# Kernel optimization log

Hardware: AMD Instinct MI355X
Metric: run time of the kernel (lower is better)

The kernel has to match this reference:

```python
import jax, jax.numpy as jnp
import numpy as np

N_USERS = 50000
N_ITEMS = 50000
E = 400000
S = 128   # in_feats_s (memory / GRU hidden)
T = 64    # in_feats_t (time encoding dim)
ED = 64   # edge feature dim
M = 2 * S + T + ED  # in_feats_m = 384

_BASIS_FREQ = jnp.asarray(1.0 / 10 ** np.linspace(0, 9, T), dtype=jnp.float32)


def time_encode(ts):
    # cos(ts * freq + phase), phase == 0
    return jnp.cos(ts[:, None] * _BASIS_FREQ[None, :])


def mean_message(src_mem, dst_mem, ts, e, src, dst, n_dst):
    # mail per edge: [E, 2S + T + ED]
    mail = jnp.concatenate(
        [src_mem[src], dst_mem[dst], time_encode(ts), e], axis=1)
    s = jax.ops.segment_sum(mail, dst, num_segments=n_dst)
    cnt = jax.ops.segment_sum(jnp.ones_like(ts), dst, num_segments=n_dst)
    return s / jnp.maximum(cnt, 1.0)[:, None]


def gru_step(x, h, w_ih, w_hh, b_ih, b_hh):
    # single-step PyTorch GRU; gate order r, z, n
    gi = x @ w_ih.T + b_ih
    gh = h @ w_hh.T + b_hh
    ir, iz, i_n = jnp.split(gi, 3, axis=1)
    hr, hz, h_n = jnp.split(gh, 3, axis=1)
    r = jax.nn.sigmoid(ir + hr)
    z = jax.nn.sigmoid(iz + hz)
    n = jnp.tanh(i_n + r * h_n)
    return (1.0 - z) * n + z * h


def setup_inputs() -> dict:
    key = jax.random.key(0)
    ks = jax.random.split(key, 16)
    sc = 1.0 / np.sqrt(S)
    return {
        "si":   jax.random.normal(ks[0], (N_USERS, S), jnp.float32),
        "sj":   jax.random.normal(ks[1], (N_ITEMS, S), jnp.float32),
        "si_r": jax.random.normal(ks[2], (N_ITEMS, S), jnp.float32),
        "sj_r": jax.random.normal(ks[3], (N_USERS, S), jnp.float32),
        "t":    jax.random.uniform(ks[4], (E,), jnp.float32),
        "t_r":  jax.random.uniform(ks[5], (E,), jnp.float32),
        "e":    jax.random.normal(ks[6], (E, ED), jnp.float32),
        "e_r":  jax.random.normal(ks[7], (E, ED), jnp.float32),
        "w_ih": jax.random.normal(ks[8], (3 * S, M), jnp.float32) * sc,
        "w_hh": jax.random.normal(ks[9], (3 * S, S), jnp.float32) * sc,
        "b_ih": jax.random.normal(ks[10], (3 * S,), jnp.float32) * sc,
        "b_hh": jax.random.normal(ks[11], (3 * S,), jnp.float32) * sc,
        "src_g":  jax.random.randint(ks[12], (E,), 0, N_USERS, jnp.int32),
        "dst_g":  jax.random.randint(ks[13], (E,), 0, N_ITEMS, jnp.int32),
        "src_gr": jax.random.randint(ks[14], (E,), 0, N_ITEMS, jnp.int32),
        "dst_gr": jax.random.randint(ks[15], (E,), 0, N_USERS, jnp.int32),
    }


def reference(si, sj, si_r, sj_r, t, t_r, e, e_r,
              w_ih, w_hh, b_ih, b_hh,
              src_g, dst_g, src_gr, dst_gr):
    # g: user -> item; g_r: item -> user
    mj = mean_message(si, sj, t, e, src_g, dst_g, N_ITEMS)       # messages to items
    mi = mean_message(si_r, sj_r, t_r, e_r, src_gr, dst_gr, N_USERS)  # messages to users
    si_out = gru_step(mi, sj_r, w_ih, w_hh, b_ih, b_hh)  # user memory update
    sj_out = gru_step(mj, sj, w_ih, w_hh, b_ih, b_hh)    # item memory update
    return (si_out, sj_out)
```

## Files before the change

### kernel.cpp

```cpp
#include <hip/hip_runtime.h>
#include <math.h>

#define NUSERS 50000
#define NITEMS 50000
#define NTOT   100000
#define NNODE  50000
#define NCHUNK 196
#define MTILES 6250
#define KDIM   512

typedef __attribute__((ext_vector_type(4))) float f32x4;
typedef __attribute__((ext_vector_type(8))) short short8;
typedef unsigned int u32;

#define AS1 __attribute__((address_space(1)))
#define AS3 __attribute__((address_space(3)))

static __device__ __forceinline__ unsigned short f2bf(float f) {
  unsigned int u = __float_as_uint(f);
  u += 0x7fffu + ((u >> 16) & 1u);
  return (unsigned short)(u >> 16);
}

static __device__ __forceinline__ void gload_lds16(const void* g, void* l) {
  __builtin_amdgcn_global_load_lds((const AS1 u32*)g, (AS3 u32*)l, 16, 0, 0);
}

__global__ void pack_w_kernel(const float* __restrict__ w_ih,
                              const float* __restrict__ w_hh,
                              const float* __restrict__ b_ih,
                              const float* __restrict__ b_hh,
                              unsigned short* __restrict__ Wb,
                              float* __restrict__ bb) {
  int idx = blockIdx.x * 256 + threadIdx.x;
  int j = idx & 7, l = (idx >> 3) & 63, ktt = idx >> 9;
  int kt = ktt & 15, tt = ktt >> 4;
  int g = tt * 16 + (l & 15);
  int k = kt * 32 + (l >> 4) * 8 + j;
  float v;
  if (g < 256)      v = (k < 384) ? w_ih[g * 384 + k] : w_hh[g * 128 + (k - 384)];
  else if (g < 384) v = (k < 384) ? w_ih[g * 384 + k] : 0.0f;
  else              v = (k < 384) ? 0.0f : w_hh[(g - 128) * 128 + (k - 384)];
  Wb[idx] = f2bf(v);
  if (idx < 512) {
    float b = (idx < 256) ? (b_ih[idx] + b_hh[idx])
            : (idx < 384) ? b_ih[idx]
                          : b_hh[idx - 128];
    bb[idx] = b;
  }
}

__global__ void hist_kernel(const int* __restrict__ dst_g,
                            const int* __restrict__ dst_gr,
                            int* __restrict__ deg_j, int* __restrict__ deg_i, int E) {
  int i = blockIdx.x * 256 + threadIdx.x;
  if (i < E) atomicAdd(&deg_j[dst_g[i]], 1);
  else if (i < 2 * E) atomicAdd(&deg_i[dst_gr[i - E]], 1);
}

__global__ void chunksum_kernel(const int* __restrict__ deg_j,
                                const int* __restrict__ deg_i,
                                int* __restrict__ csum) {
  int c = blockIdx.x;
  const int* deg = (c < NCHUNK) ? deg_j : deg_i;
  int cc = (c < NCHUNK) ? c : c - NCHUNK;
  int t = threadIdx.x;
  int idx = cc * 256 + t;
  int v = (idx < NNODE) ? deg[idx] : 0;
  for (int off = 32; off; off >>= 1) v += __shfl_down(v, off, 64);
  __shared__ int wsum[4];
  if ((t & 63) == 0) wsum[t >> 6] = v;
  __syncthreads();
  if (t == 0) csum[c] = wsum[0] + wsum[1] + wsum[2] + wsum[3];
}

__global__ void chunkscan_kernel(const int* __restrict__ csum, int* __restrict__ coff) {
  int d = blockIdx.x;
  const int* cs = csum + d * NCHUNK;
  int* co = coff + d * NCHUNK;
  int t = threadIdx.x, lane = t & 63, w = t >> 6;
  int v = (t < NCHUNK) ? cs[t] : 0;
  int x = v;
  for (int off = 1; off < 64; off <<= 1) {
    int y = __shfl_up(x, off, 64);
    if (lane >= off) x += y;
  }
  __shared__ int wt[4];
  if (lane == 63) wt[w] = x;
  __syncthreads();
  int add = 0;
  for (int k = 0; k < 4; ++k) if (k < w) add += wt[k];
  if (t < NCHUNK) co[t] = add + x - v;
}

__global__ void localscan_kernel(const int* __restrict__ deg_j,
                                 const int* __restrict__ deg_i,
                                 const int* __restrict__ coff,
                                 int* __restrict__ rs_j, int* __restrict__ cur_j,
                                 int* __restrict__ rs_i, int* __restrict__ cur_i) {
  int c = blockIdx.x;
  bool dj = c < NCHUNK;
  const int* deg = dj ? deg_j : deg_i;
  int cc = dj ? c : c - NCHUNK;
  int* rs = dj ? rs_j : rs_i;
  int* cur = dj ? cur_j : cur_i;
  int base = coff[c];
  int t = threadIdx.x, lane = t & 63, w = t >> 6;
  int idx = cc * 256 + t;
  int v = (idx < NNODE) ? deg[idx] : 0;
  int x = v;
  for (int off = 1; off < 64; off <<= 1) {
    int y = __shfl_up(x, off, 64);
    if (lane >= off) x += y;
  }
  __shared__ int wt[4];
  if (lane == 63) wt[w] = x;
  __syncthreads();
  int add = 0;
  for (int k = 0; k < 4; ++k) if (k < w) add += wt[k];
  int ex = base + add + x - v;
  if (idx < NNODE) { rs[idx] = ex; cur[idx] = ex; }
}

__global__ void fill_kernel(const int* __restrict__ src_g, const int* __restrict__ dst_g,
                            const float* __restrict__ t,
                            const int* __restrict__ src_gr, const int* __restrict__ dst_gr,
                            const float* __restrict__ t_r,
                            int* __restrict__ cur_j, int* __restrict__ cur_i,
                            int4* __restrict__ recP_j, int4* __restrict__ recP_i,
                            int E) {
  int i = blockIdx.x * 256 + threadIdx.x;
  if (i < E) {
    int pos = atomicAdd(&cur_j[dst_g[i]], 1);
    recP_j[pos] = make_int4(src_g[i], i, __float_as_int(t[i]), 0);
  } else if (i < 2 * E) {
    int k = i - E;
    int pos = atomicAdd(&cur_i[dst_gr[k]], 1);
    recP_i[pos] = make_int4(src_gr[k], k, __float_as_int(t_r[k]), 0);
  }
}

__global__ __launch_bounds__(256) void gather_kernel(
    const float* __restrict__ si, const float* __restrict__ sj,
    const float* __restrict__ si_r, const float* __restrict__ sj_r,
    const float* __restrict__ e, const float* __restrict__ e_r,
    const int* __restrict__ rs_j, const int* __restrict__ rs_i,
    const int* __restrict__ deg_j, const int* __restrict__ deg_i,
    const int4* __restrict__ recP_j, const int4* __restrict__ recP_i,
    unsigned short* __restrict__ Xb) {
  __shared__ __align__(16) unsigned short rowbuf[4][512];
  int wid = threadIdx.x >> 6, lane = threadIdx.x & 63;
  int node = blockIdx.x * 4 + wid;
  bool user = node < NUSERS;
  int idx = user ? node : node - NUSERS;
  const float* smem = user ? si_r : si;
  const float* h    = user ? sj_r : sj;
  const float* ef   = user ? e_r : e;
  int start = __builtin_amdgcn_readfirstlane((user ? rs_i : rs_j)[idx]);
  int deg   = __builtin_amdgcn_readfirstlane((user ? deg_i : deg_j)[idx]);
  const int4* rec = user ? recP_i : recP_j;

  float freq = __expf((float)lane * -0.3289407276f);
  float a0 = 0.f, a1 = 0.f, a2 = 0.f, a3 = 0.f;

  for (int i = 0; i < deg; i += 4) {
    int i1 = (i + 1 < deg) ? i + 1 : deg - 1;
    int i2 = (i + 2 < deg) ? i + 2 : deg - 1;
    int i3 = (i + 3 < deg) ? i + 3 : deg - 1;
    int4 r0 = rec[start + i];
    int4 r1 = rec[start + i1];
    int4 r2 = rec[start + i2];
    int4 r3 = rec[start + i3];
    float w1 = (i + 1 < deg) ? 1.0f : 0.0f;
    float w2 = (i + 2 < deg) ? 1.0f : 0.0f;
    float w3 = (i + 3 < deg) ? 1.0f : 0.0f;

    float x00 = smem[(size_t)r0.x * 128 + lane];
    float x01 = smem[(size_t)r0.x * 128 + 64 + lane];
    float f0  = ef[(size_t)r0.y * 64 + lane];
    float x10 = smem[(size_t)r1.x * 128 + lane];
    float x11 = smem[(size_t)r1.x * 128 + 64 + lane];
    float f1  = ef[(size_t)r1.y * 64 + lane];
    float x20 = smem[(size_t)r2.x * 128 + lane];
    float x21 = smem[(size_t)r2.x * 128 + 64 + lane];
    float f2  = ef[(size_t)r2.y * 64 + lane];
    float x30 = smem[(size_t)r3.x * 128 + lane];
    float x31 = smem[(size_t)r3.x * 128 + 64 + lane];
    float f3  = ef[(size_t)r3.y * 64 + lane];

    float c0 = __cosf(__int_as_float(r0.z) * freq);
    float c1 = __cosf(__int_as_float(r1.z) * freq);
    float c2 = __cosf(__int_as_float(r2.z) * freq);
    float c3 = __cosf(__int_as_float(r3.z) * freq);

    a0 += x00 + w1 * x10 + w2 * x20 + w3 * x30;
    a1 += x01 + w1 * x11 + w2 * x21 + w3 * x31;
    a2 += c0  + w1 * c1  + w2 * c2  + w3 * c3;
    a3 += f0  + w1 * f1  + w2 * f2  + w3 * f3;
  }

  float invc = (deg > 0) ? 1.0f / (float)deg : 0.0f;
  float hz   = (deg > 0) ? 1.0f : 0.0f;
  float h0 = h[(size_t)idx * 128 + lane];
  float h1 = h[(size_t)idx * 128 + 64 + lane];

  unsigned short* rb = rowbuf[wid];
  rb[lane]        = f2bf(a0 * invc);
  rb[64  + lane]  = f2bf(a1 * invc);
  rb[128 + lane]  = f2bf(h0 * hz);
  rb[192 + lane]  = f2bf(h1 * hz);
  rb[256 + lane]  = f2bf(a2 * invc);
  rb[320 + lane]  = f2bf(a3 * invc);
  rb[384 + lane]  = f2bf(h0);
  rb[448 + lane]  = f2bf(h1);
  __syncthreads();

  int rt = node >> 4, m = node & 15;
  int kt = lane >> 2, q = lane & 3;
  short8 vv = *(const short8*)(rb + lane * 8);
  *(short8*)(Xb + (((size_t)rt * 16 + kt) * 64 + q * 16 + m) * 8) = vv;
}

__global__ __launch_bounds__(512, 2) void gemm_gru_kernel(
    const unsigned short* __restrict__ Xb,
    const unsigned short* __restrict__ Wb,
    const float* __restrict__ bb,
    const float* __restrict__ sj_r,
    const float* __restrict__ sj,
    float* __restrict__ out) {
  __shared__ __align__(16) unsigned short sB[32768];
  int wid = threadIdx.x >> 6, lane = threadIdx.x & 63;
  int mtile = blockIdx.x * 8 + wid;
  bool valid = mtile < MTILES;
  int col16 = lane & 15, quad = lane >> 4;

  f32x4 acc[32];
#pragma unroll
  for (int t = 0; t < 32; ++t) acc[t] = (f32x4)0.0f;

  const unsigned short* Abase = Xb + (size_t)(valid ? mtile : 0) * 8192;

  for (int s = 0; s < 8; ++s) {
#pragma unroll
    for (int i = 0; i < 8; ++i) {
      int c = wid * 8 + i;
      int tt = c >> 1, kt = s * 2 + (c & 1);
      const unsigned short* g = Wb + ((size_t)(tt * 16 + kt) * 64 + lane) * 8;
      gload_lds16(g, sB + c * 512);
    }
    __syncthreads();
    if (valid) {
      short8 a0 = *(const short8*)(Abase + (size_t)(s * 2) * 512 + lane * 8);
      short8 a1 = *(const short8*)(Abase + (size_t)(s * 2 + 1) * 512 + lane * 8);
#pragma unroll
      for (int t = 0; t < 32; ++t) {
        short8 b0 = *(const short8*)(sB + (t * 2) * 512 + lane * 8);
        short8 b1 = *(const short8*)(sB + (t * 2 + 1) * 512 + lane * 8);
        acc[t] = __builtin_amdgcn_mfma_f32_16x16x32_bf16(a0, b0, acc[t], 0, 0, 0);
        acc[t] = __builtin_amdgcn_mfma_f32_16x16x32_bf16(a1, b1, acc[t], 0, 0, 0);
      }
    }
    __syncthreads();
  }

  if (!valid) return;
  int m0 = mtile * 16;
#pragma unroll
  for (int t = 0; t < 8; ++t) {
    int c = t * 16 + col16;
    float bbr = bb[c], bbz = bb[128 + c], bbn = bb[256 + c], bbh = bb[384 + c];
#pragma unroll
    for (int r = 0; r < 4; ++r) {
      int row = m0 + quad * 4 + r;
      float rp  = acc[t][r]      + bbr;
      float zp  = acc[t + 8][r]  + bbz;
      float inp = acc[t + 16][r] + bbn;
      float hnp = acc[t + 24][r] + bbh;
      float rg = 1.0f / (1.0f + __expf(-rp));
      float zg = 1.0f / (1.0f + __expf(-zp));
      float ng = tanhf(inp + rg * hnp);
      float hv = (row < NUSERS) ? sj_r[(size_t)row * 128 + c]
                                : sj[(size_t)(row - NUSERS) * 128 + c];
      out[(size_t)row * 128 + c] = (1.0f - zg) * ng + zg * hv;
    }
  }
}

extern "C" void kernel_launch(void* const* d_in, const int* in_sizes, int n_in,
                              void* d_out, int out_size, void* d_ws, size_t ws_size,
                              hipStream_t stream) {
  const float* si   = (const float*)d_in[0];
  const float* sj   = (const float*)d_in[1];
  const float* si_r = (const float*)d_in[2];
  const float* sj_r = (const float*)d_in[3];
  const float* t    = (const float*)d_in[4];
  const float* t_r  = (const float*)d_in[5];
  const float* e    = (const float*)d_in[6];
  const float* e_r  = (const float*)d_in[7];
  const float* w_ih = (const float*)d_in[8];
  const float* w_hh = (const float*)d_in[9];
  const float* b_ih = (const float*)d_in[10];
  const float* b_hh = (const float*)d_in[11];
  const int* src_g  = (const int*)d_in[12];
  const int* dst_g  = (const int*)d_in[13];
  const int* src_gr = (const int*)d_in[14];
  const int* dst_gr = (const int*)d_in[15];
  int E = in_sizes[4];

  unsigned short* Xb = (unsigned short*)d_ws;
  unsigned short* Wb = Xb + (size_t)MTILES * 8192;
  float* bb   = (float*)(Wb + 262144);
  int* deg_j  = (int*)(bb + 512);
  int* deg_i  = deg_j + NNODE;
  int* rs_j   = deg_i + NNODE;
  int* rs_i   = rs_j + NNODE;
  int* cur_j  = rs_i + NNODE;
  int* cur_i  = cur_j + NNODE;
  int* csum   = cur_i + NNODE;
  int* coff   = csum + 2 * NCHUNK;
  int4* recP_j = (int4*)(coff + 2 * NCHUNK);
  int4* recP_i = recP_j + E;

  hipMemsetAsync(deg_j, 0, 2 * NNODE * sizeof(int), stream);

  pack_w_kernel<<<(512 * 512) / 256, 256, 0, stream>>>(w_ih, w_hh, b_ih, b_hh, Wb, bb);

  int blks2E = (2 * E + 255) / 256;
  hist_kernel<<<blks2E, 256, 0, stream>>>(dst_g, dst_gr, deg_j, deg_i, E);
  chunksum_kernel<<<2 * NCHUNK, 256, 0, stream>>>(deg_j, deg_i, csum);
  chunkscan_kernel<<<2, 256, 0, stream>>>(csum, coff);
  localscan_kernel<<<2 * NCHUNK, 256, 0, stream>>>(deg_j, deg_i, coff, rs_j, cur_j, rs_i, cur_i);
  fill_kernel<<<blks2E, 256, 0, stream>>>(src_g, dst_g, t, src_gr, dst_gr, t_r,
                                          cur_j, cur_i, recP_j, recP_i, E);

  gather_kernel<<<NTOT / 4, 256, 0, stream>>>(si, sj, si_r, sj_r, e, e_r,
                                              rs_j, rs_i, deg_j, deg_i,
                                              recP_j, recP_i, Xb);

  float* out = (float*)d_out;
  gemm_gru_kernel<<<(MTILES + 7) / 8, 512, 0, stream>>>(Xb, Wb, bb, sj_r, sj, out);
}
```

Measured before the change: 656.9 us.

## Vectorize edge gather with 16-byte loads and wave-wide record prefetch

Restructures the per-node gather loop so each wave loads up to 64 edge records at once and broadcasts them with readlane. Instead of one scalar float per lane per row, it issues 16-byte vector loads, so each half-wave reads a different source-memory row and each quarter-wave a different edge-feature row, eight edges per iteration. Partial sums are combined across lanes with xor shuffles before conversion to bf16. This is meant to cut the number of memory instructions and raise memory-level parallelism, at the cost of extra shuffles, lane selection logic and wasted lanes on low-degree nodes.

New measurement: 656.9 us. No clear change (+0.0%).

```diff
diff --git a/kernel.cpp b/kernel.cpp
--- a/kernel.cpp
+++ b/kernel.cpp
@@ -156,63 +156,97 @@
   const float* smem = user ? si_r : si;
   const float* h    = user ? sj_r : sj;
   const float* ef   = user ? e_r : e;
-  int start = __builtin_amdgcn_readfirstlane((user ? rs_i : rs_j)[idx]);
-  int deg   = __builtin_amdgcn_readfirstlane((user ? deg_i : deg_j)[idx]);
+  int start = (user ? rs_i : rs_j)[idx];
+  int deg   = (user ? deg_i : deg_j)[idx];
   const int4* rec = user ? recP_i : recP_j;
 
+  int half = lane >> 5, l32 = lane & 31;
+  int quar = lane >> 4, l16 = lane & 15;
   float freq = __expf((float)lane * -0.3289407276f);
-  float a0 = 0.f, a1 = 0.f, a2 = 0.f, a3 = 0.f;
-
-  for (int i = 0; i < deg; i += 4) {
-    int i1 = (i + 1 < deg) ? i + 1 : deg - 1;
-    int i2 = (i + 2 < deg) ? i + 2 : deg - 1;
-    int i3 = (i + 3 < deg) ? i + 3 : deg - 1;
-    int4 r0 = rec[start + i];
-    int4 r1 = rec[start + i1];
-    int4 r2 = rec[start + i2];
-    int4 r3 = rec[start + i3];
-    float w1 = (i + 1 < deg) ? 1.0f : 0.0f;
-    float w2 = (i + 2 < deg) ? 1.0f : 0.0f;
-    float w3 = (i + 3 < deg) ? 1.0f : 0.0f;
-
-    float x00 = smem[(size_t)r0.x * 128 + lane];
-    float x01 = smem[(size_t)r0.x * 128 + 64 + lane];
-    float f0  = ef[(size_t)r0.y * 64 + lane];
-    float x10 = smem[(size_t)r1.x * 128 + lane];
-    float x11 = smem[(size_t)r1.x * 128 + 64 + lane];
-    float f1  = ef[(size_t)r1.y * 64 + lane];
-    float x20 = smem[(size_t)r2.x * 128 + lane];
-    float x21 = smem[(size_t)r2.x * 128 + 64 + lane];
-    float f2  = ef[(size_t)r2.y * 64 + lane];
-    float x30 = smem[(size_t)r3.x * 128 + lane];
-    float x31 = smem[(size_t)r3.x * 128 + 64 + lane];
-    float f3  = ef[(size_t)r3.y * 64 + lane];
-
-    float c0 = __cosf(__int_as_float(r0.z) * freq);
-    float c1 = __cosf(__int_as_float(r1.z) * freq);
-    float c2 = __cosf(__int_as_float(r2.z) * freq);
-    float c3 = __cosf(__int_as_float(r3.z) * freq);
-
-    a0 += x00 + w1 * x10 + w2 * x20 + w3 * x30;
-    a1 += x01 + w1 * x11 + w2 * x21 + w3 * x31;
-    a2 += c0  + w1 * c1  + w2 * c2  + w3 * c3;
-    a3 += f0  + w1 * f1  + w2 * f2  + w3 * f3;
+
+  f32x4 accS = {0.f, 0.f, 0.f, 0.f};
+  f32x4 accE = {0.f, 0.f, 0.f, 0.f};
+  float accT = 0.f;
+
+  for (int c0 = 0; c0 < deg; c0 += 64) {
+    int nrec = min(64, deg - c0);
+    int rlx = 0, rly = 0, rlz = 0;
+    if (lane < nrec) {
+      int4 r = rec[start + c0 + lane];
+      rlx = r.x; rly = r.y; rlz = r.z;
+    }
+    for (int i = 0; i < nrec; i += 8) {
+      int srow[8], erow[8];
+      float tsv[8], wj[8];
+#pragma unroll
+      for (int j = 0; j < 8; ++j) {
+        int ei = i + j;
+        int eidx = (ei < nrec) ? ei : nrec - 1;
+        wj[j] = (ei < nrec) ? 1.0f : 0.0f;
+        srow[j] = __builtin_amdgcn_readlane(rlx, eidx);
+        erow[j] = __builtin_amdgcn_readlane(rly, eidx);
+        tsv[j]  = __int_as_float(__builtin_amdgcn_readlane(rlz, eidx));
+      }
+      f32x4 sv[4]; float sw[4];
+#pragma unroll
+      for (int p = 0; p < 4; ++p) {
+        int rsel = half ? srow[2 * p + 1] : srow[2 * p];
+        sw[p]    = half ? wj[2 * p + 1]   : wj[2 * p];
+        sv[p] = *(const f32x4*)(smem + (size_t)rsel * 128 + l32 * 4);
+      }
+      f32x4 ev[2]; float ew[2];
+#pragma unroll
+      for (int p = 0; p < 2; ++p) {
+        int b = 4 * p;
+        int rlo = (quar & 1) ? erow[b + 1] : erow[b];
+        int rhi = (quar & 1) ? erow[b + 3] : erow[b + 2];
+        int rsel = (quar & 2) ? rhi : rlo;
+        float wlo = (quar & 1) ? wj[b + 1] : wj[b];
+        float whi = (quar & 1) ? wj[b + 3] : wj[b + 2];
+        ew[p] = (quar & 2) ? whi : wlo;
+        ev[p] = *(const f32x4*)(ef + (size_t)rsel * 64 + l16 * 4);
+      }
+#pragma unroll
+      for (int j = 0; j < 8; ++j)
+        accT += wj[j] * __cosf(tsv[j] * freq);
+#pragma unroll
+      for (int p = 0; p < 4; ++p) accS += sv[p] * sw[p];
+#pragma unroll
+      for (int p = 0; p < 2; ++p) accE += ev[p] * ew[p];
+    }
+  }
+
+#pragma unroll
+  for (int k = 0; k < 4; ++k) {
+    accS[k] += __shfl_xor(accS[k], 32);
+    float t1 = accE[k] + __shfl_xor(accE[k], 32);
+    accE[k] = t1 + __shfl_xor(t1, 16);
   }
 
   float invc = (deg > 0) ? 1.0f / (float)deg : 0.0f;
   float hz   = (deg > 0) ? 1.0f : 0.0f;
-  float h0 = h[(size_t)idx * 128 + lane];
-  float h1 = h[(size_t)idx * 128 + 64 + lane];
+  f32x4 hv = *(const f32x4*)(h + (size_t)idx * 128 + l32 * 4);
 
   unsigned short* rb = rowbuf[wid];
-  rb[lane]        = f2bf(a0 * invc);
-  rb[64  + lane]  = f2bf(a1 * invc);
-  rb[128 + lane]  = f2bf(h0 * hz);
-  rb[192 + lane]  = f2bf(h1 * hz);
-  rb[256 + lane]  = f2bf(a2 * invc);
-  rb[320 + lane]  = f2bf(a3 * invc);
-  rb[384 + lane]  = f2bf(h0);
-  rb[448 + lane]  = f2bf(h1);
+  if (half == 0) {
+    ushort4 s4, h4a, h4b;
+    s4.x = f2bf(accS[0] * invc); s4.y = f2bf(accS[1] * invc);
+    s4.z = f2bf(accS[2] * invc); s4.w = f2bf(accS[3] * invc);
+    h4a.x = f2bf(hv[0] * hz); h4a.y = f2bf(hv[1] * hz);
+    h4a.z = f2bf(hv[2] * hz); h4a.w = f2bf(hv[3] * hz);
+    h4b.x = f2bf(hv[0]); h4b.y = f2bf(hv[1]);
+    h4b.z = f2bf(hv[2]); h4b.w = f2bf(hv[3]);
+    *(ushort4*)(rb + 4 * l32)       = s4;
+    *(ushort4*)(rb + 128 + 4 * l32) = h4a;
+    *(ushort4*)(rb + 384 + 4 * l32) = h4b;
+  }
+  rb[256 + lane] = f2bf(accT * invc);
+  if (lane < 16) {
+    ushort4 e4;
+    e4.x = f2bf(accE[0] * invc); e4.y = f2bf(accE[1] * invc);
+    e4.z = f2bf(accE[2] * invc); e4.w = f2bf(accE[3] * invc);
+    *(ushort4*)(rb + 320 + 4 * l16) = e4;
+  }
   __syncthreads();
 
   int rt = node >> 4, m = node & 15;
```
